# Kernel optimization log

Hardware: AMD Instinct MI355X
Metric: run time of the kernel (lower is better)

The kernel has to match this reference:

```python
import jax, jax.numpy as jnp
import numpy as np

B, C = 8, 256
GRID = 128          # H = W = grid_size
N = GRID * GRID     # 16384 tokens
WS = 8              # swin window size
NH = 8              # num heads
DH = C // NH        # head dim = 32
HID = int(C * 4.0)  # mlp hidden = 1024
EPS = 1e-5


def _ln(x, g, b):
    m = jnp.mean(x, axis=-1, keepdims=True)
    v = jnp.mean(jnp.square(x - m), axis=-1, keepdims=True)
    return (x - m) * jax.lax.rsqrt(v + EPS) * g + b


def setup_inputs() -> dict:
    key = jax.random.key(0)
    ks = jax.random.split(key, 6)
    s = 0.02
    return {
        "x": jax.random.normal(ks[0], (B, N, C), jnp.float32),
        "ln1_g": jnp.ones((C,), jnp.float32), "ln1_b": jnp.zeros((C,), jnp.float32),
        "in_w": jax.random.normal(ks[1], (3 * C, C), jnp.float32) * s,
        "in_b": jnp.zeros((3 * C,), jnp.float32),
        "out_w": jax.random.normal(ks[2], (C, C), jnp.float32) * s,
        "out_b": jnp.zeros((C,), jnp.float32),
        "ln2_g": jnp.ones((C,), jnp.float32), "ln2_b": jnp.zeros((C,), jnp.float32),
        "w1": jax.random.normal(ks[3], (HID, C), jnp.float32) * s,
        "b1": jnp.zeros((HID,), jnp.float32),
        "w2": jax.random.normal(ks[4], (C, HID), jnp.float32) * s,
        "b2": jnp.zeros((C,), jnp.float32),
    }


def reference(x, ln1_g, ln1_b, in_w, in_b, out_w, out_b, ln2_g, ln2_b, w1, b1, w2, b2):
    shortcut = x
    xn = _ln(x, ln1_g, ln1_b)
    # window partition: [B,N,C] -> [B,H,W,C] -> [B*nW, WS*WS, C]
    xw = (xn.reshape(B, GRID // WS, WS, GRID // WS, WS, C)
            .transpose(0, 1, 3, 2, 4, 5)
            .reshape(-1, WS * WS, C))
    # torch nn.MultiheadAttention: fused in-proj, scale 1/sqrt(head_dim)
    qkv = xw @ in_w.T + in_b                      # [nW, T, 3C]
    q, k, v = jnp.split(qkv, 3, axis=-1)
    def heads(t):
        return t.reshape(t.shape[0], t.shape[1], NH, DH).transpose(0, 2, 1, 3)
    q, k, v = heads(q), heads(k), heads(v)        # [nW, NH, T, DH]
    scores = jnp.einsum('whtd,whsd->whts', q, k) * (1.0 / np.sqrt(DH))
    att = jax.nn.softmax(scores, axis=-1)
    o = jnp.einsum('whts,whsd->whtd', att, v)     # [nW, NH, T, DH]
    o = o.transpose(0, 2, 1, 3).reshape(-1, WS * WS, C)
    o = o @ out_w.T + out_b
    # window reverse: [B*nW, WS, WS, C] -> [B, N, C]
    x_attn = (o.reshape(B, GRID // WS, GRID // WS, WS, WS, C)
                .transpose(0, 1, 3, 2, 4, 5)
                .reshape(B, N, C))
    x = shortcut + x_attn
    h = _ln(x, ln2_g, ln2_b)
    h = jax.nn.gelu(h @ w1.T + b1, approximate=False)  # torch nn.GELU = exact erf
    return x + h @ w2.T + b2
```

## Files before the change

### kernel.cpp

```cpp
#include <hip/hip_runtime.h>
#include <hip/hip_bf16.h>
#include <cstdint>

#define DEVINL __device__ __forceinline__

using bf16 = __hip_bfloat16;
typedef __bf16 bf16x8 __attribute__((ext_vector_type(8)));
typedef float f32x4 __attribute__((ext_vector_type(4)));

static constexpr int MTOK = 131072;

DEVINL void async_ld16(const void* g, void* l) {
  __builtin_amdgcn_global_load_lds(
      (__attribute__((address_space(1))) void*)(g),
      (__attribute__((address_space(3))) void*)(l), 16, 0, 0);
}

DEVINL unsigned short bfbits(float v) {
  bf16 h = __float2bfloat16(v);
  return *reinterpret_cast<unsigned short*>(&h);
}

__global__ __launch_bounds__(256) void cvt_w(
    const float* __restrict__ w0, const float* __restrict__ w1,
    const float* __restrict__ w2, const float* __restrict__ w3,
    bf16* __restrict__ out) {
  int i = blockIdx.x * 256 + threadIdx.x;
  float v;
  if (i < 196608)      v = w0[i];
  else if (i < 262144) v = w1[i - 196608];
  else if (i < 524288) v = w2[i - 262144];
  else                 v = w3[i - 524288];
  out[i] = __float2bfloat16(v);
}

template <bool REMAP>
__global__ __launch_bounds__(256) void ln_kern(
    const float* __restrict__ x, const float* __restrict__ gw,
    const float* __restrict__ bw, bf16* __restrict__ out) {
  const int lane = threadIdx.x & 63;
  const int wv = threadIdx.x >> 6;
  const long tok = (long)blockIdx.x * 4 + wv;
  const float4 v = *(const float4*)(x + tok * 256 + lane * 4);
  float s = v.x + v.y + v.z + v.w;
#pragma unroll
  for (int off = 32; off > 0; off >>= 1) s += __shfl_xor(s, off);
  const float mean = s * (1.0f / 256.0f);
  const float dx = v.x - mean, dy = v.y - mean, dz = v.z - mean, dw = v.w - mean;
  float q = dx * dx + dy * dy + dz * dz + dw * dw;
#pragma unroll
  for (int off = 32; off > 0; off >>= 1) q += __shfl_xor(q, off);
  const float inv = rsqrtf(q * (1.0f / 256.0f) + 1e-5f);
  long drow;
  if (REMAP) {
    const int b = (int)(tok >> 14);
    const int n = (int)(tok & 16383);
    const int row = n >> 7, col = n & 127;
    const int w = b * 256 + (row >> 3) * 16 + (col >> 3);
    const int t = (row & 7) * 8 + (col & 7);
    drow = ((long)w * 64 + t) * 256;
  } else {
    drow = tok * 256;
  }
  const float4 g = *(const float4*)(gw + lane * 4);
  const float4 bb = *(const float4*)(bw + lane * 4);
  ushort4 o;
  o.x = bfbits(dx * inv * g.x + bb.x);
  o.y = bfbits(dy * inv * g.y + bb.y);
  o.z = bfbits(dz * inv * g.z + bb.z);
  o.w = bfbits(dw * inv * g.w + bb.w);
  *(ushort4*)((unsigned short*)out + drow + lane * 4) = o;
}

enum { EPI_QKV = 0, EPI_OUTPROJ = 1, EPI_GELU = 2, EPI_RESID = 3 };

template <int K, int EPI>
__global__ __launch_bounds__(256) void gemm_db(
    const bf16* __restrict__ A, const bf16* __restrict__ Bw,
    const float* __restrict__ bias,
    bf16* __restrict__ oQ, bf16* __restrict__ oK, bf16* __restrict__ oV,
    const float* __restrict__ resid, float* __restrict__ of32,
    bf16* __restrict__ obf, int ldo) {
  __shared__ __align__(16) unsigned short As[2][128 * 64];
  __shared__ __align__(16) unsigned short Bs[2][128 * 64];
  const int tid = threadIdx.x;
  const int lane = tid & 63, wv = tid >> 6;
  const int quad = lane >> 4, l16 = lane & 15;
  const int wm = wv >> 1, wn = wv & 1;
  const long m0 = (long)blockIdx.x * 128;
  const int n0 = blockIdx.y * 128;

  auto stage = [&](int i, int buf) {
    const int k0 = i * 64;
#pragma unroll
    for (int p = 0; p < 4; ++p) {
      const int f = p * 256 + tid;
      const int row = f >> 3;
      const int c8 = (f & 7) ^ (row & 7);
      async_ld16(A + (m0 + row) * K + (k0 + c8 * 8), (char*)&As[buf][0] + f * 16);
      async_ld16(Bw + (long)(n0 + row) * K + (k0 + c8 * 8), (char*)&Bs[buf][0] + f * 16);
    }
  };

  const f32x4 fz = {0.f, 0.f, 0.f, 0.f};
  f32x4 acc[4][4];
#pragma unroll
  for (int a = 0; a < 4; ++a) {
#pragma unroll
    for (int b = 0; b < 4; ++b) acc[a][b] = fz;
  }

  constexpr int NI = K / 64;
  stage(0, 0);
#pragma unroll 1
  for (int i = 0; i < NI; ++i) {
    __builtin_amdgcn_s_waitcnt(0x0F70);
    __builtin_amdgcn_sched_barrier(0);
    __builtin_amdgcn_s_barrier();
    __builtin_amdgcn_sched_barrier(0);
    if (i + 1 < NI) stage(i + 1, (i + 1) & 1);
    const unsigned short* Asb = &As[i & 1][0];
    const unsigned short* Bsb = &Bs[i & 1][0];
#pragma unroll
    for (int kk = 0; kk < 2; ++kk) {
      bf16x8 af[4], bfr[4];
#pragma unroll
      for (int mt = 0; mt < 4; ++mt) {
        const int row = wm * 64 + mt * 16 + l16;
        const int c8 = (kk * 4 + quad) ^ (row & 7);
        af[mt] = *(const bf16x8*)(Asb + row * 64 + c8 * 8);
      }
#pragma unroll
      for (int nt = 0; nt < 4; ++nt) {
        const int row = wn * 64 + nt * 16 + l16;
        const int c8 = (kk * 4 + quad) ^ (row & 7);
        bfr[nt] = *(const bf16x8*)(Bsb + row * 64 + c8 * 8);
      }
#pragma unroll
      for (int mt = 0; mt < 4; ++mt) {
#pragma unroll
        for (int nt = 0; nt < 4; ++nt) {
          acc[mt][nt] = __builtin_amdgcn_mfma_f32_16x16x32_bf16(
              af[mt], bfr[nt], acc[mt][nt], 0, 0, 0);
        }
      }
    }
  }

#pragma unroll
  for (int mt = 0; mt < 4; ++mt) {
#pragma unroll
    for (int nt = 0; nt < 4; ++nt) {
      const long mb = m0 + wm * 64 + mt * 16 + quad * 4;
      const int j = n0 + wn * 64 + nt * 16 + l16;
      const float bj = bias[j];
#pragma unroll
      for (int r = 0; r < 4; ++r) {
        const long m = mb + r;
        const float v = acc[mt][nt][r] + bj;
        if constexpr (EPI == EPI_QKV) {
          const int w = (int)(m >> 6), t = (int)(m & 63);
          const int region = j >> 8, hh = (j >> 5) & 7, d = j & 31;
          const long hb = (long)w * 8 + hh;
          if (region == 0)      oQ[(hb * 64 + t) * 32 + d] = __float2bfloat16(v);
          else if (region == 1) oK[(hb * 64 + t) * 32 + d] = __float2bfloat16(v);
          else                  oV[(hb * 32 + d) * 64 + t] = __float2bfloat16(v);
        } else if constexpr (EPI == EPI_OUTPROJ) {
          const int w = (int)(m >> 6), t = (int)(m & 63);
          const int b = w >> 8, wi = w & 255;
          const int row = (wi >> 4) * 8 + (t >> 3);
          const int col = (wi & 15) * 8 + (t & 7);
          const long addr = ((long)b * 16384 + row * 128 + col) * 256 + j;
          of32[addr] = v + resid[addr];
        } else if constexpr (EPI == EPI_GELU) {
          const float g = 0.5f * v * (1.0f + erff(v * 0.70710678118654752f));
          obf[m * (long)ldo + j] = __float2bfloat16(g);
        } else {
          const long addr = m * 256 + j;
          of32[addr] += v;
        }
      }
    }
  }
}

__global__ __launch_bounds__(256) void attn_kern(
    const bf16* __restrict__ Qb, const bf16* __restrict__ Kb,
    const bf16* __restrict__ Vtb, bf16* __restrict__ O) {
  __shared__ __align__(16) unsigned short P[4][64 * 72];
  const int lane = threadIdx.x & 63;
  const int wv = threadIdx.x >> 6;
  const int quad = lane >> 4, l16 = lane & 15;
  const long w = blockIdx.x;
  unsigned short* Pw = &P[wv][0];
  const float SC = 0.17677669529663689f;
  const f32x4 fz = {0.f, 0.f, 0.f, 0.f};

#pragma unroll 1
  for (int hi = 0; hi < 2; ++hi) {
    const int h = wv * 2 + hi;
    const bf16* qp = Qb + ((w * 8 + h) * 64) * 32;
    const bf16* kp = Kb + ((w * 8 + h) * 64) * 32;
    const bf16* vt = Vtb + ((w * 8 + h) * 32) * 64;

    bf16x8 qf[4], kf[4];
#pragma unroll
    for (int mt = 0; mt < 4; ++mt)
      qf[mt] = *(const bf16x8*)(qp + (mt * 16 + l16) * 32 + quad * 8);
#pragma unroll
    for (int nt = 0; nt < 4; ++nt)
      kf[nt] = *(const bf16x8*)(kp + (nt * 16 + l16) * 32 + quad * 8);

    f32x4 s[4][4];
#pragma unroll
    for (int a = 0; a < 4; ++a) {
#pragma unroll
      for (int b = 0; b < 4; ++b) s[a][b] = fz;
    }
#pragma unroll
    for (int mt = 0; mt < 4; ++mt) {
#pragma unroll
      for (int nt = 0; nt < 4; ++nt) {
        s[mt][nt] = __builtin_amdgcn_mfma_f32_16x16x32_bf16(qf[mt], kf[nt],
                                                            s[mt][nt], 0, 0, 0);
      }
    }

#pragma unroll
    for (int mt = 0; mt < 4; ++mt) {
#pragma unroll
      for (int r = 0; r < 4; ++r) {
        float a0 = s[mt][0][r] * SC, a1 = s[mt][1][r] * SC;
        float a2 = s[mt][2][r] * SC, a3 = s[mt][3][r] * SC;
        float mx = fmaxf(fmaxf(a0, a1), fmaxf(a2, a3));
#pragma unroll
        for (int off = 8; off > 0; off >>= 1) mx = fmaxf(mx, __shfl_xor(mx, off));
        a0 = __expf(a0 - mx); a1 = __expf(a1 - mx);
        a2 = __expf(a2 - mx); a3 = __expf(a3 - mx);
        float sm = a0 + a1 + a2 + a3;
#pragma unroll
        for (int off = 8; off > 0; off >>= 1) sm += __shfl_xor(sm, off);
        const float iv = 1.0f / sm;
        const int rp = (mt * 16 + quad * 4 + r) * 72;
        Pw[rp + l16]      = bfbits(a0 * iv);
        Pw[rp + 16 + l16] = bfbits(a1 * iv);
        Pw[rp + 32 + l16] = bfbits(a2 * iv);
        Pw[rp + 48 + l16] = bfbits(a3 * iv);
      }
    }

    bf16x8 vf[2][2];
#pragma unroll
    for (int kt = 0; kt < 2; ++kt) {
#pragma unroll
      for (int dt = 0; dt < 2; ++dt)
        vf[kt][dt] = *(const bf16x8*)(vt + (dt * 16 + l16) * 64 + kt * 32 + quad * 8);
    }
    f32x4 oa[4][2];
#pragma unroll
    for (int a = 0; a < 4; ++a) { oa[a][0] = fz; oa[a][1] = fz; }
#pragma unroll
    for (int mt = 0; mt < 4; ++mt) {
      const unsigned short* pr = Pw + (mt * 16 + l16) * 72 + quad * 8;
      const bf16x8 p0 = *(const bf16x8*)(pr);
      const bf16x8 p1 = *(const bf16x8*)(pr + 32);
#pragma unroll
      for (int dt = 0; dt < 2; ++dt) {
        oa[mt][dt] = __builtin_amdgcn_mfma_f32_16x16x32_bf16(p0, vf[0][dt], oa[mt][dt], 0, 0, 0);
        oa[mt][dt] = __builtin_amdgcn_mfma_f32_16x16x32_bf16(p1, vf[1][dt], oa[mt][dt], 0, 0, 0);
      }
    }

#pragma unroll
    for (int mt = 0; mt < 4; ++mt) {
#pragma unroll
      for (int dt = 0; dt < 2; ++dt) {
#pragma unroll
        for (int r = 0; r < 4; ++r) {
          O[(w * 64 + mt * 16 + quad * 4 + r) * 256 + h * 32 + dt * 16 + l16] =
              __float2bfloat16(oa[mt][dt][r]);
        }
      }
    }
  }
}

extern "C" void kernel_launch(void* const* d_in, const int* in_sizes, int n_in,
                              void* d_out, int out_size, void* d_ws, size_t ws_size,
                              hipStream_t stream) {
  const float* x     = (const float*)d_in[0];
  const float* ln1g  = (const float*)d_in[1];
  const float* ln1b  = (const float*)d_in[2];
  const float* in_w  = (const float*)d_in[3];
  const float* in_b  = (const float*)d_in[4];
  const float* out_w = (const float*)d_in[5];
  const float* out_b = (const float*)d_in[6];
  const float* ln2g  = (const float*)d_in[7];
  const float* ln2b  = (const float*)d_in[8];
  const float* w1    = (const float*)d_in[9];
  const float* b1    = (const float*)d_in[10];
  const float* w2    = (const float*)d_in[11];
  const float* b2    = (const float*)d_in[12];
  float* out = (float*)d_out;

  char* ws = (char*)d_ws;
  const size_t MB = 1ull << 20;
  bf16* Wc   = (bf16*)ws;
  bf16* Wqkv = Wc;
  bf16* Wo   = Wc + 196608;
  bf16* W1c  = Wc + 262144;
  bf16* W2c  = Wc + 524288;
  bf16* XW   = (bf16*)(ws + 2 * MB);
  bf16* Qb   = (bf16*)(ws + 66 * MB);
  bf16* Kb   = (bf16*)(ws + 130 * MB);
  bf16* Vtb  = (bf16*)(ws + 194 * MB);
  bf16* H1   = (bf16*)(ws + 66 * MB);
  bf16* Obuf = XW;
  bf16* Hbuf = XW;

  cvt_w<<<3072, 256, 0, stream>>>(in_w, out_w, w1, w2, Wc);
  ln_kern<true><<<MTOK / 4, 256, 0, stream>>>(x, ln1g, ln1b, XW);
  gemm_db<256, EPI_QKV><<<dim3(MTOK / 128, 6), 256, 0, stream>>>(
      XW, Wqkv, in_b, Qb, Kb, Vtb, nullptr, nullptr, nullptr, 0);
  attn_kern<<<2048, 256, 0, stream>>>(Qb, Kb, Vtb, Obuf);
  gemm_db<256, EPI_OUTPROJ><<<dim3(MTOK / 128, 2), 256, 0, stream>>>(
      Obuf, Wo, out_b, nullptr, nullptr, nullptr, x, out, nullptr, 0);
  ln_kern<false><<<MTOK / 4, 256, 0, stream>>>(out, ln2g, ln2b, Hbuf);
  gemm_db<256, EPI_GELU><<<dim3(MTOK / 128, 8), 256, 0, stream>>>(
      Hbuf, W1c, b1, nullptr, nullptr, nullptr, nullptr, nullptr, H1, 1024);
  gemm_db<1024, EPI_RESID><<<dim3(MTOK / 128, 2), 256, 0, stream>>>(
      H1, W2c, b2, nullptr, nullptr, nullptr, nullptr, out, nullptr, 0);
}
```

Before: 941.9 us.

## Store GEMM operands in pre-swizzled contiguous tile panels and swap grid order

Every producer (weight conversion, layernorm, attention output, GELU epilogue) now writes its bf16 operand in a packed layout of 128-row by 64-column panels with the LDS XOR swizzle already applied. Each GEMM stage then loads one contiguous 16 KB block instead of strided rows. The grid is also transposed so consecutive blocks share the same M tile across N tiles, which should improve L2 reuse of the A panel. The cost is scattered 2-byte writes in the GELU and attention epilogues, which may hurt write coalescing.

```diff
diff --git a/kernel.cpp b/kernel.cpp
--- a/kernel.cpp
+++ b/kernel.cpp
@@ -19,6 +19,14 @@
 DEVINL unsigned short bfbits(float v) {
   bf16 h = __float2bfloat16(v);
   return *reinterpret_cast<unsigned short*>(&h);
+}
+
+DEVINL long pkaddr(long m, int k, int KP) {
+  const long tile = m >> 7;
+  const int row = (int)(m & 127);
+  const int panel = k >> 6;
+  const int c8 = ((k & 63) >> 3) ^ (row & 7);
+  return ((tile * KP + panel) * 1024 + row * 8 + c8) * 8 + (k & 7);
 }
 
 __global__ __launch_bounds__(256) void cvt_w(
@@ -26,12 +34,12 @@
     const float* __restrict__ w2, const float* __restrict__ w3,
     bf16* __restrict__ out) {
   int i = blockIdx.x * 256 + threadIdx.x;
-  float v;
-  if (i < 196608)      v = w0[i];
-  else if (i < 262144) v = w1[i - 196608];
-  else if (i < 524288) v = w2[i - 262144];
-  else                 v = w3[i - 524288];
-  out[i] = __float2bfloat16(v);
+  float v; long base; int n, k, KP;
+  if (i < 196608)       { v = w0[i]; base = 0;      n = i / 256;  k = i & 255;  KP = 4; }
+  else if (i < 262144)  { int j = i - 196608; v = w1[j]; base = 196608; n = j / 256; k = j & 255; KP = 4; }
+  else if (i < 524288)  { int j = i - 262144; v = w2[j]; base = 262144; n = j / 256; k = j & 255; KP = 4; }
+  else                  { int j = i - 524288; v = w3[j]; base = 524288; n = j >> 10; k = j & 1023; KP = 16; }
+  out[base + pkaddr(n, k, KP)] = __float2bfloat16(v);
 }
 
 template <bool REMAP>
@@ -51,16 +59,16 @@
 #pragma unroll
   for (int off = 32; off > 0; off >>= 1) q += __shfl_xor(q, off);
   const float inv = rsqrtf(q * (1.0f / 256.0f) + 1e-5f);
-  long drow;
+  long m;
   if (REMAP) {
     const int b = (int)(tok >> 14);
     const int n = (int)(tok & 16383);
     const int row = n >> 7, col = n & 127;
     const int w = b * 256 + (row >> 3) * 16 + (col >> 3);
     const int t = (row & 7) * 8 + (col & 7);
-    drow = ((long)w * 64 + t) * 256;
+    m = (long)w * 64 + t;
   } else {
-    drow = tok * 256;
+    m = tok;
   }
   const float4 g = *(const float4*)(gw + lane * 4);
   const float4 bb = *(const float4*)(bw + lane * 4);
@@ -69,36 +77,37 @@
   o.y = bfbits(dy * inv * g.y + bb.y);
   o.z = bfbits(dz * inv * g.z + bb.z);
   o.w = bfbits(dw * inv * g.w + bb.w);
-  *(ushort4*)((unsigned short*)out + drow + lane * 4) = o;
+  *(ushort4*)((unsigned short*)out + pkaddr(m, lane * 4, 4)) = o;
 }
 
 enum { EPI_QKV = 0, EPI_OUTPROJ = 1, EPI_GELU = 2, EPI_RESID = 3 };
 
-template <int K, int EPI>
+template <int KP, int EPI>
 __global__ __launch_bounds__(256) void gemm_db(
     const bf16* __restrict__ A, const bf16* __restrict__ Bw,
     const float* __restrict__ bias,
     bf16* __restrict__ oQ, bf16* __restrict__ oK, bf16* __restrict__ oV,
     const float* __restrict__ resid, float* __restrict__ of32,
-    bf16* __restrict__ obf, int ldo) {
+    bf16* __restrict__ obf) {
   __shared__ __align__(16) unsigned short As[2][128 * 64];
   __shared__ __align__(16) unsigned short Bs[2][128 * 64];
   const int tid = threadIdx.x;
   const int lane = tid & 63, wv = tid >> 6;
   const int quad = lane >> 4, l16 = lane & 15;
   const int wm = wv >> 1, wn = wv & 1;
-  const long m0 = (long)blockIdx.x * 128;
-  const int n0 = blockIdx.y * 128;
+  const int ntile = blockIdx.x;
+  const long mtile = blockIdx.y;
+  const long m0 = mtile * 128;
+  const int n0 = ntile * 128;
 
   auto stage = [&](int i, int buf) {
-    const int k0 = i * 64;
+    const bf16* Apan = A + (mtile * KP + i) * 8192;
+    const bf16* Bpan = Bw + ((long)ntile * KP + i) * 8192;
 #pragma unroll
     for (int p = 0; p < 4; ++p) {
       const int f = p * 256 + tid;
-      const int row = f >> 3;
-      const int c8 = (f & 7) ^ (row & 7);
-      async_ld16(A + (m0 + row) * K + (k0 + c8 * 8), (char*)&As[buf][0] + f * 16);
-      async_ld16(Bw + (long)(n0 + row) * K + (k0 + c8 * 8), (char*)&Bs[buf][0] + f * 16);
+      async_ld16(Apan + f * 8, (char*)&As[buf][0] + f * 16);
+      async_ld16(Bpan + f * 8, (char*)&Bs[buf][0] + f * 16);
     }
   };
 
@@ -110,15 +119,14 @@
     for (int b = 0; b < 4; ++b) acc[a][b] = fz;
   }
 
-  constexpr int NI = K / 64;
   stage(0, 0);
 #pragma unroll 1
-  for (int i = 0; i < NI; ++i) {
+  for (int i = 0; i < KP; ++i) {
     __builtin_amdgcn_s_waitcnt(0x0F70);
     __builtin_amdgcn_sched_barrier(0);
     __builtin_amdgcn_s_barrier();
     __builtin_amdgcn_sched_barrier(0);
-    if (i + 1 < NI) stage(i + 1, (i + 1) & 1);
+    if (i + 1 < KP) stage(i + 1, (i + 1) & 1);
     const unsigned short* Asb = &As[i & 1][0];
     const unsigned short* Bsb = &Bs[i & 1][0];
 #pragma unroll
@@ -174,7 +182,7 @@
           of32[addr] = v + resid[addr];
         } else if constexpr (EPI == EPI_GELU) {
           const float g = 0.5f * v * (1.0f + erff(v * 0.70710678118654752f));
-          obf[m * (long)ldo + j] = __float2bfloat16(g);
+          obf[pkaddr(m, j, 16)] = __float2bfloat16(g);
         } else {
           const long addr = m * 256 + j;
           of32[addr] += v;
@@ -277,8 +285,9 @@
       for (int dt = 0; dt < 2; ++dt) {
 #pragma unroll
         for (int r = 0; r < 4; ++r) {
-          O[(w * 64 + mt * 16 + quad * 4 + r) * 256 + h * 32 + dt * 16 + l16] =
-              __float2bfloat16(oa[mt][dt][r]);
+          const long m = w * 64 + mt * 16 + quad * 4 + r;
+          const int k = h * 32 + dt * 16 + l16;
+          O[pkaddr(m, k, 4)] = __float2bfloat16(oa[mt][dt][r]);
         }
       }
     }
@@ -320,14 +329,14 @@
 
   cvt_w<<<3072, 256, 0, stream>>>(in_w, out_w, w1, w2, Wc);
   ln_kern<true><<<MTOK / 4, 256, 0, stream>>>(x, ln1g, ln1b, XW);
-  gemm_db<256, EPI_QKV><<<dim3(MTOK / 128, 6), 256, 0, stream>>>(
-      XW, Wqkv, in_b, Qb, Kb, Vtb, nullptr, nullptr, nullptr, 0);
+  gemm_db<4, EPI_QKV><<<dim3(6, MTOK / 128), 256, 0, stream>>>(
+      XW, Wqkv, in_b, Qb, Kb, Vtb, nullptr, nullptr, nullptr);
   attn_kern<<<2048, 256, 0, stream>>>(Qb, Kb, Vtb, Obuf);
-  gemm_db<256, EPI_OUTPROJ><<<dim3(MTOK / 128, 2), 256, 0, stream>>>(
-      Obuf, Wo, out_b, nullptr, nullptr, nullptr, x, out, nullptr, 0);
+  gemm_db<4, EPI_OUTPROJ><<<dim3(2, MTOK / 128), 256, 0, stream>>>(
+      Obuf, Wo, out_b, nullptr, nullptr, nullptr, x, out, nullptr);
   ln_kern<false><<<MTOK / 4, 256, 0, stream>>>(out, ln2g, ln2b, Hbuf);
-  gemm_db<256, EPI_GELU><<<dim3(MTOK / 128, 8), 256, 0, stream>>>(
-      Hbuf, W1c, b1, nullptr, nullptr, nullptr, nullptr, nullptr, H1, 1024);
-  gemm_db<1024, EPI_RESID><<<dim3(MTOK / 128, 2), 256, 0, stream>>>(
-      H1, W2c, b2, nullptr, nullptr, nullptr, nullptr, out, nullptr, 0);
-}
+  gemm_db<4, EPI_GELU><<<dim3(8, MTOK / 128), 256, 0, stream>>>(
+      Hbuf, W1c, b1, nullptr, nullptr, nullptr, nullptr, nullptr, H1);
+  gemm_db<16, EPI_RESID><<<dim3(2, MTOK / 128), 256, 0, stream>>>(
+      H1, W2c, b2, nullptr, nullptr, nullptr, nullptr, out, nullptr);
+}
```

Result: faster. 887.4 us (-5.8%).
